# Kernel tuning notes

Measured on AMD Instinct MI355X. Metric: run time of the kernel, lower is better.

## Reference

```python
import jax, jax.numpy as jnp
import numpy as np

L, D, H, V, B, S = 12, 768, 12, 50257, 1, 2048
F = 4 * D
HD = D // H
EPS = 1e-5
NEG = -1e38


def setup_inputs() -> dict:
    key = jax.random.key(0)
    ks = jax.random.split(key, 12)
    s = 0.02
    f32 = jnp.float32
    return {
        "x": jax.random.normal(ks[0], (B, S, D), f32),
        "ln1_g": jnp.ones((L, D), f32), "ln1_b": jnp.zeros((L, D), f32),
        "Wq": jax.random.normal(ks[1], (L, D, D), f32) * s,
        "Wk": jax.random.normal(ks[2], (L, D, D), f32) * s,
        "Wv": jax.random.normal(ks[3], (L, D, D), f32) * s,
        "Wo": jax.random.normal(ks[4], (L, D, D), f32) * s,
        "bo": jnp.zeros((L, D), f32),
        "ln2_g": jnp.ones((L, D), f32), "ln2_b": jnp.zeros((L, D), f32),
        "Wfc": jax.random.normal(ks[5], (L, D, F), f32) * s,
        "bfc": jnp.zeros((L, F), f32),
        "Wp": jax.random.normal(ks[6], (L, F, D), f32) * s,
        "bp": jnp.zeros((L, D), f32),
        "lnf_g": jnp.ones((D,), f32), "lnf_b": jnp.zeros((D,), f32),
        "Wlm": jax.random.normal(ks[7], (D, V), f32) * s,
    }


def _ln(h, g, b):
    mu = h.mean(-1, keepdims=True)
    var = ((h - mu) ** 2).mean(-1, keepdims=True)
    return (h - mu) * jax.lax.rsqrt(var + EPS) * g + b


def reference(x, ln1_g, ln1_b, Wq, Wk, Wv, Wo, bo, ln2_g, ln2_b,
              Wfc, bfc, Wp, bp, lnf_g, lnf_b, Wlm):
    Bx, Sx, Dx = x.shape
    # additive causal mask, NOTE: original has no 1/sqrt(head_dim) scaling
    mask = (1.0 - jnp.tril(jnp.ones((Sx, Sx), x.dtype))) * NEG

    def block(h, p):
        g1, b1, wq, wk, wv, wo, bo_, g2, b2, wfc, bfc_, wp, bp_ = p
        hn = _ln(h, g1, b1)
        def heads(w):  # [B,S,D] -> [B,H,S,hd]
            return (hn @ w).reshape(Bx, Sx, H, HD).transpose(0, 2, 1, 3)
        q, k, v = heads(wq), heads(wk), heads(wv)
        scores = jnp.einsum('bhqd,bhkd->bhqk', q, k) + mask
        probs = jax.nn.softmax(scores, axis=-1)
        attn = jnp.einsum('bhqk,bhkd->bhqd', probs, v)
        attn = attn.transpose(0, 2, 1, 3).reshape(Bx, Sx, Dx)
        h = h + attn @ wo + bo_
        hn2 = _ln(h, g2, b2)
        ff = jax.nn.gelu(hn2 @ wfc + bfc_, approximate=False) @ wp + bp_
        return h + ff, None

    h, _ = jax.lax.scan(
        block, x,
        (ln1_g, ln1_b, Wq, Wk, Wv, Wo, bo, ln2_g, ln2_b, Wfc, bfc, Wp, bp))
    return _ln(h, lnf_g, lnf_b) @ Wlm
```

## Files before the change

kernel.cpp:

```cpp
#include <hip/hip_runtime.h>
#include <hip/hip_bf16.h>
#include <math.h>

typedef unsigned short ushort;
typedef __attribute__((ext_vector_type(8))) short short8;
typedef __attribute__((ext_vector_type(4))) short short4v;
typedef __attribute__((ext_vector_type(4))) float f4v;

constexpr int SEQ = 2048;
constexpr int DM  = 768;
constexpr int NH  = 12;
constexpr int HDM = 64;
constexpr int FF  = 3072;
constexpr int NL  = 12;
constexpr int NV  = 50257;
constexpr int NVP = 50304;

__device__ inline ushort f2bf(float f) {
    union { float f; unsigned u; } v; v.f = f;
    unsigned r = v.u + 0x7fffu + ((v.u >> 16) & 1u);
    return (ushort)(r >> 16);
}

__device__ __forceinline__ void gld16(const ushort* g, ushort* l) {
    __builtin_amdgcn_global_load_lds(
        (const __attribute__((address_space(1))) void*)g,
        (__attribute__((address_space(3))) void*)l, 16, 0, 0);
}

__global__ __launch_bounds__(256) void ln_kernel(const float* __restrict__ x,
                                                 const float* __restrict__ g,
                                                 const float* __restrict__ b,
                                                 ushort* __restrict__ out) {
    int row = blockIdx.x;
    int t = threadIdx.x;
    const float* xr = x + (size_t)row * DM;
    float v0 = xr[t], v1 = xr[t + 256], v2 = xr[t + 512];
    float s = v0 + v1 + v2;
    float s2 = v0 * v0 + v1 * v1 + v2 * v2;
    for (int m = 1; m < 64; m <<= 1) { s += __shfl_xor(s, m); s2 += __shfl_xor(s2, m); }
    __shared__ float ls[4], ls2[4];
    int w = t >> 6;
    if ((t & 63) == 0) { ls[w] = s; ls2[w] = s2; }
    __syncthreads();
    s = ls[0] + ls[1] + ls[2] + ls[3];
    s2 = ls2[0] + ls2[1] + ls2[2] + ls2[3];
    float mu = s * (1.0f / DM);
    float var = s2 * (1.0f / DM) - mu * mu;
    float rs = rsqrtf(var + 1e-5f);
    ushort* o = out + (size_t)row * DM;
    o[t]       = f2bf((v0 - mu) * rs * g[t]       + b[t]);
    o[t + 256] = f2bf((v1 - mu) * rs * g[t + 256] + b[t + 256]);
    o[t + 512] = f2bf((v2 - mu) * rs * g[t + 512] + b[t + 512]);
}

__global__ __launch_bounds__(256) void cvt_t(const float* __restrict__ in, size_t inL,
                                             ushort* __restrict__ out, size_t outL,
                                             int K, int N) {
    __shared__ ushort T[64][72];
    int l = blockIdx.z;
    const float* ip = in + (size_t)l * inL;
    ushort* op = out + (size_t)l * outL;
    int kb = blockIdx.x * 64, nb = blockIdx.y * 64;
    int t = threadIdx.x;
    int nl = t & 63, ks = (t >> 6) * 16;
    int n = nb + nl;
    #pragma unroll
    for (int j = 0; j < 16; ++j) {
        float f = (n < N) ? ip[(size_t)(kb + ks + j) * N + n] : 0.f;
        T[nl][ks + j] = f2bf(f);
    }
    __syncthreads();
    int r = t >> 2, c4 = (t & 3) * 16;
    *(short8*)(op + (size_t)(nb + r) * K + kb + c4)     = *(const short8*)&T[r][c4];
    *(short8*)(op + (size_t)(nb + r) * K + kb + c4 + 8) = *(const short8*)&T[r][c4 + 8];
}

template <int BM, int BN, int EPI, bool DB>
__global__ __launch_bounds__(256) void gemmT(const ushort* __restrict__ A,
                                             const ushort* __restrict__ Bt,
                                             const float* __restrict__ bias,
                                             const float* __restrict__ res,
                                             void* __restrict__ outp,
                                             ushort* __restrict__ vt,
                                             int M, int N, int K, int ldOut) {
    constexpr int FM = BM / 32;
    constexpr int FN = BN / 32;
    constexpr int NBUF = DB ? 2 : 1;
    constexpr int ASZ = BM * 64;
    constexpr int BSZ = BN * 64;
    __shared__ ushort As[NBUF * ASZ];
    __shared__ ushort Bs[NBUF * BSZ];
    int tid = threadIdx.x, lane = tid & 63, wave = tid >> 6;
    int wm = (wave >> 1) * (BM / 2), wn = (wave & 1) * (BN / 2);
    int mBase = blockIdx.x * BM, nBase = blockIdx.y * BN;
    int lr = lane & 15, lg = lane >> 4;
    int swz = (lr & 7) << 3;

    f4v acc[FM][FN];
    #pragma unroll
    for (int i = 0; i < FM; ++i)
        #pragma unroll
        for (int j = 0; j < FN; ++j) acc[i][j] = (f4v){0.f, 0.f, 0.f, 0.f};

    int cBase = wave * 64 + lane;

    auto stage = [&](int kb, int buf) {
        #pragma unroll
        for (int i = 0; i < BM / 32; ++i) {
            int c = i * 256 + cBase;
            int row = c >> 3;
            int kc = (c & 7) ^ (row & 7);
            gld16(A + (size_t)(mBase + row) * K + kb + kc * 8,
                  As + buf * ASZ + (size_t)(i * 256 + wave * 64) * 8);
        }
        #pragma unroll
        for (int i = 0; i < BN / 32; ++i) {
            int c = i * 256 + cBase;
            int row = c >> 3;
            int kc = (c & 7) ^ (row & 7);
            gld16(Bt + (size_t)(nBase + row) * K + kb + kc * 8,
                  Bs + buf * BSZ + (size_t)(i * 256 + wave * 64) * 8);
        }
    };
    auto compute = [&](int buf) {
        #pragma unroll
        for (int kk = 0; kk < 2; ++kk) {
            short8 a[FM], b[FN];
            #pragma unroll
            for (int fr = 0; fr < FM; ++fr)
                a[fr] = *(const short8*)(As + buf * ASZ + (wm + fr * 16 + lr) * 64 + ((((kk * 4 + lg) << 3)) ^ swz));
            #pragma unroll
            for (int fc = 0; fc < FN; ++fc)
                b[fc] = *(const short8*)(Bs + buf * BSZ + (wn + fc * 16 + lr) * 64 + ((((kk * 4 + lg) << 3)) ^ swz));
            #pragma unroll
            for (int fr = 0; fr < FM; ++fr)
                #pragma unroll
                for (int fc = 0; fc < FN; ++fc)
                    acc[fr][fc] = __builtin_amdgcn_mfma_f32_16x16x32_bf16(a[fr], b[fc], acc[fr][fc], 0, 0, 0);
        }
    };

    if constexpr (DB) {
        stage(0, 0);
        __syncthreads();
        int cur = 0;
        for (int kb = 0; kb < K; kb += 64) {
            if (kb + 64 < K) stage(kb + 64, cur ^ 1);
            compute(cur);
            __syncthreads();
            cur ^= 1;
        }
    } else {
        for (int kb = 0; kb < K; kb += 64) {
            stage(kb, 0);
            __syncthreads();
            compute(0);
            __syncthreads();
        }
    }

    if constexpr (EPI == 4) {
        if (nBase < 1536) {
            #pragma unroll
            for (int fr = 0; fr < FM; ++fr)
                #pragma unroll
                for (int fc = 0; fc < FN; ++fc)
                    #pragma unroll
                    for (int r = 0; r < 4; ++r) {
                        int row = mBase + wm + fr * 16 + 4 * lg + r;
                        int col = nBase + wn + fc * 16 + lr;
                        ((ushort*)outp)[(size_t)row * ldOut + col] = f2bf(acc[fr][fc][r]);
                    }
        } else {
            #pragma unroll
            for (int fr = 0; fr < FM; ++fr)
                #pragma unroll
                for (int fc = 0; fc < FN; ++fc) {
                    short4v pk;
                    #pragma unroll
                    for (int r = 0; r < 4; ++r) pk[r] = (short)f2bf(acc[fr][fc][r]);
                    int d  = nBase - 1536 + wn + fc * 16 + lr;
                    int m0 = mBase + wm + fr * 16 + 4 * lg;
                    *(short4v*)(vt + (size_t)d * SEQ + m0) = pk;
                }
        }
        return;
    }

    #pragma unroll
    for (int fr = 0; fr < FM; ++fr)
        #pragma unroll
        for (int fc = 0; fc < FN; ++fc)
            #pragma unroll
            for (int r = 0; r < 4; ++r) {
                int row = mBase + wm + fr * 16 + 4 * lg + r;
                int col = nBase + wn + fc * 16 + lr;
                float v = acc[fr][fc][r];
                if constexpr (EPI == 0) {
                    ((ushort*)outp)[(size_t)row * ldOut + col] = f2bf(v);
                } else if constexpr (EPI == 1) {
                    v += bias[col] + res[(size_t)row * ldOut + col];
                    ((float*)outp)[(size_t)row * ldOut + col] = v;
                } else if constexpr (EPI == 2) {
                    v += bias[col];
                    v = 0.5f * v * (1.f + erff(v * 0.70710678118f));
                    ((ushort*)outp)[(size_t)row * ldOut + col] = f2bf(v);
                } else {
                    if (col < N) ((float*)outp)[(size_t)row * ldOut + col] = v;
                }
            }
}

__global__ __launch_bounds__(256) void attn_v6(const ushort* __restrict__ Qg,
                                               const ushort* __restrict__ Kg,
                                               const ushort* __restrict__ Vt,
                                               ushort* __restrict__ Og) {
    __shared__ ushort Ks[2 * 4096];
    __shared__ ushort Vs[2 * 4096];
    __shared__ ushort Ps[4 * 16 * 64];
    int tid = threadIdx.x, lane = tid & 63, wave = tid >> 6;
    int flat = blockIdx.x;
    int qb   = (SEQ / 64) - 1 - (flat / NH);
    int head = flat % NH;
    int lr = lane & 15, lg = lane >> 4;
    int qr0 = qb * 64 + wave * 16;
    int hoff = head * HDM;
    int swz = (lr & 7) << 3;

    short8 qf0 = *(const short8*)(Qg + (size_t)(qr0 + lr) * 2304 + hoff + lg * 8);
    short8 qf1 = *(const short8*)(Qg + (size_t)(qr0 + lr) * 2304 + hoff + 32 + lg * 8);

    const f4v fz = {0.f, 0.f, 0.f, 0.f};
    f4v o[4];
    o[0] = fz; o[1] = fz; o[2] = fz; o[3] = fz;
    float mrow[4] = {-1e30f, -1e30f, -1e30f, -1e30f};
    float lsum[4] = {0.f, 0.f, 0.f, 0.f};

    int c0 = wave * 64 + lane;
    int c1 = c0 + 256;
    int r0 = c0 >> 3, kc0 = ((c0 & 7) ^ (r0 & 7)) * 8;
    int r1 = c1 >> 3, kc1 = ((c1 & 7) ^ (r1 & 7)) * 8;

    auto stageKV = [&](int kb, int buf) {
        gld16(Kg + (size_t)(kb * 64 + r0) * 2304 + hoff + kc0, Ks + buf * 4096 + wave * 512);
        gld16(Kg + (size_t)(kb * 64 + r1) * 2304 + hoff + kc1, Ks + buf * 4096 + 2048 + wave * 512);
        gld16(Vt + (size_t)(hoff + r0) * SEQ + kb * 64 + kc0,  Vs + buf * 4096 + wave * 512);
        gld16(Vt + (size_t)(hoff + r1) * SEQ + kb * 64 + kc1,  Vs + buf * 4096 + 2048 + wave * 512);
    };

    stageKV(0, 0);
    __syncthreads();
    int cur = 0;

    for (int kb = 0; kb <= qb; ++kb) {
        if (kb < qb) stageKV(kb + 1, cur ^ 1);

        f4v s[4];
        #pragma unroll
        for (int n = 0; n < 4; ++n) {
            const ushort* kr = Ks + cur * 4096 + (n * 16 + lr) * 64;
            short8 k0 = *(const short8*)(kr + ((lg << 3) ^ swz));
            short8 k1 = *(const short8*)(kr + ((((4 + lg) << 3)) ^ swz));
            f4v z = fz;
            z = __builtin_amdgcn_mfma_f32_16x16x32_bf16(qf0, k0, z, 0, 0, 0);
            s[n] = __builtin_amdgcn_mfma_f32_16x16x32_bf16(qf1, k1, z, 0, 0, 0);
        }
        if (kb == qb) {
            #pragma unroll
            for (int n = 0; n < 4; ++n)
                #pragma unroll
                for (int r = 0; r < 4; ++r) {
                    int col = kb * 64 + n * 16 + lr;
                    int row = qr0 + 4 * lg + r;
                    if (col > row) s[n][r] = -1e38f;
                }
        }

        int sub = lr & 7, hi = lr >> 3;
        #pragma unroll
        for (int r = 0; r < 4; ++r) {
            float mx = fmaxf(fmaxf(s[0][r], s[1][r]), fmaxf(s[2][r], s[3][r]));
            mx = fmaxf(mx, __shfl_xor(mx, 1));
            mx = fmaxf(mx, __shfl_xor(mx, 2));
            mx = fmaxf(mx, __shfl_xor(mx, 4));
            mx = fmaxf(mx, __shfl_xor(mx, 8));
            float mnew = fmaxf(mrow[r], mx);
            float corr = __expf(mrow[r] - mnew);
            float ps0 = __expf(s[0][r] - mnew);
            float ps1 = __expf(s[1][r] - mnew);
            float ps2 = __expf(s[2][r] - mnew);
            float ps3 = __expf(s[3][r] - mnew);
            float rs = ps0 + ps1 + ps2 + ps3;
            rs += __shfl_xor(rs, 1);
            rs += __shfl_xor(rs, 2);
            rs += __shfl_xor(rs, 4);
            rs += __shfl_xor(rs, 8);
            lsum[r] = lsum[r] * corr + rs;
            mrow[r] = mnew;
            o[0][r] *= corr; o[1][r] *= corr; o[2][r] *= corr; o[3][r] *= corr;
            int prow = 4 * lg + r;
            ushort* pb = Ps + wave * 1024 + prow * 64;
            int px = prow & 7;
            pb[(((0 + hi) ^ px) << 3) | sub] = f2bf(ps0);
            pb[(((2 + hi) ^ px) << 3) | sub] = f2bf(ps1);
            pb[(((4 + hi) ^ px) << 3) | sub] = f2bf(ps2);
            pb[(((6 + hi) ^ px) << 3) | sub] = f2bf(ps3);
        }
        __syncthreads();

        #pragma unroll
        for (int kk = 0; kk < 2; ++kk) {
            short8 pa = *(const short8*)(Ps + wave * 1024 + lr * 64 + ((((kk * 4 + lg) << 3)) ^ swz));
            #pragma unroll
            for (int dn = 0; dn < 4; ++dn) {
                short8 vb = *(const short8*)(Vs + cur * 4096 + (dn * 16 + lr) * 64 + ((((kk * 4 + lg) << 3)) ^ swz));
                o[dn] = __builtin_amdgcn_mfma_f32_16x16x32_bf16(pa, vb, o[dn], 0, 0, 0);
            }
        }
        __syncthreads();
        cur ^= 1;
    }

    #pragma unroll
    for (int dn = 0; dn < 4; ++dn)
        #pragma unroll
        for (int r = 0; r < 4; ++r) {
            int row = qr0 + 4 * lg + r;
            Og[(size_t)row * DM + hoff + dn * 16 + lr] = f2bf(o[dn][r] / lsum[r]);
        }
}

template <int EPI>
__global__ __launch_bounds__(256) void gemm64(const ushort* __restrict__ A,
                                              const float* __restrict__ B,
                                              const float* __restrict__ bias,
                                              const float* __restrict__ res,
                                              void* __restrict__ outp,
                                              int M, int N, int K) {
    __shared__ ushort As[64][64];
    __shared__ ushort Bs[64][72];
    int tid = threadIdx.x;
    int lane = tid & 63, wave = tid >> 6;
    int wm = (wave >> 1) * 32, wn = (wave & 1) * 32;
    int mBase = blockIdx.x * 64, nBase = blockIdx.y * 64;
    int lr = lane & 15, lg = lane >> 4;

    const f4v fz = {0.f, 0.f, 0.f, 0.f};
    f4v acc[2][2];
    acc[0][0] = fz; acc[0][1] = fz; acc[1][0] = fz; acc[1][1] = fz;

    int ar = tid >> 2, ac = (tid & 3) * 16;
    int br = tid >> 2, bc = (tid & 3) * 16;

    for (int kb = 0; kb < K; kb += 64) {
        const short8* ag = (const short8*)(A + (size_t)(mBase + ar) * K + kb + ac);
        *(short8*)&As[ar][ac]     = ag[0];
        *(short8*)&As[ar][ac + 8] = ag[1];
        if constexpr (EPI == 3) {
            #pragma unroll
            for (int j = 0; j < 16; ++j) {
                int col = nBase + bc + j;
                float f = (col < N) ? B[(size_t)(kb + br) * N + col] : 0.f;
                Bs[bc + j][br] = f2bf(f);
            }
        } else {
            const float4* bg = (const float4*)(B + (size_t)(kb + br) * N + nBase + bc);
            float fv[16];
            *(float4*)&fv[0]  = bg[0];
            *(float4*)&fv[4]  = bg[1];
            *(float4*)&fv[8]  = bg[2];
            *(float4*)&fv[12] = bg[3];
            #pragma unroll
            for (int j = 0; j < 16; ++j) Bs[bc + j][br] = f2bf(fv[j]);
        }
        __syncthreads();
        #pragma unroll
        for (int kk = 0; kk < 2; ++kk) {
            short8 a0 = *(const short8*)&As[wm + lr][kk * 32 + lg * 8];
            short8 a1 = *(const short8*)&As[wm + 16 + lr][kk * 32 + lg * 8];
            short8 b0 = *(const short8*)&Bs[wn + lr][kk * 32 + lg * 8];
            short8 b1 = *(const short8*)&Bs[wn + 16 + lr][kk * 32 + lg * 8];
            acc[0][0] = __builtin_amdgcn_mfma_f32_16x16x32_bf16(a0, b0, acc[0][0], 0, 0, 0);
            acc[0][1] = __builtin_amdgcn_mfma_f32_16x16x32_bf16(a0, b1, acc[0][1], 0, 0, 0);
            acc[1][0] = __builtin_amdgcn_mfma_f32_16x16x32_bf16(a1, b0, acc[1][0], 0, 0, 0);
            acc[1][1] = __builtin_amdgcn_mfma_f32_16x16x32_bf16(a1, b1, acc[1][1], 0, 0, 0);
        }
        __syncthreads();
    }

    #pragma unroll
    for (int fm = 0; fm < 2; ++fm)
        #pragma unroll
        for (int fn = 0; fn < 2; ++fn)
            #pragma unroll
            for (int r = 0; r < 4; ++r) {
                int row = mBase + wm + fm * 16 + 4 * lg + r;
                int col = nBase + wn + fn * 16 + lr;
                float v = acc[fm][fn][r];
                if constexpr (EPI == 0) {
                    ((ushort*)outp)[(size_t)row * N + col] = f2bf(v);
                } else if constexpr (EPI == 1) {
                    v += bias[col] + res[(size_t)row * N + col];
                    ((float*)outp)[(size_t)row * N + col] = v;
                } else if constexpr (EPI == 2) {
                    v += bias[col];
                    v = 0.5f * v * (1.f + erff(v * 0.70710678118f));
                    ((ushort*)outp)[(size_t)row * N + col] = f2bf(v);
                } else {
                    if (col < N) ((float*)outp)[(size_t)row * N + col] = v;
                }
            }
}

__global__ __launch_bounds__(256) void attn_stage(const ushort* __restrict__ Qg,
                                                  const ushort* __restrict__ Kg,
                                                  const ushort* __restrict__ Vg,
                                                  ushort* __restrict__ Og,
                                                  int ld) {
    __shared__ ushort Ks[64][64];
    __shared__ ushort Vs[64][72];
    __shared__ ushort Ps[4][16][64];
    int tid = threadIdx.x, lane = tid & 63, wave = tid >> 6;
    int qb = blockIdx.x, head = blockIdx.y;
    int lr = lane & 15, lg = lane >> 4;
    int qr0 = qb * 64 + wave * 16;
    size_t hoff = (size_t)head * HDM;

    short8 qf0 = *(const short8*)(Qg + (size_t)(qr0 + lr) * ld + hoff + lg * 8);
    short8 qf1 = *(const short8*)(Qg + (size_t)(qr0 + lr) * ld + hoff + 32 + lg * 8);

    const f4v fz = {0.f, 0.f, 0.f, 0.f};
    f4v o[4];
    o[0] = fz; o[1] = fz; o[2] = fz; o[3] = fz;
    float mrow[4] = {-1e30f, -1e30f, -1e30f, -1e30f};
    float lsum[4] = {0.f, 0.f, 0.f, 0.f};

    int r_ = tid >> 2, c_ = (tid & 3) * 16;

    for (int kb = 0; kb <= qb; ++kb) {
        const short8* kg = (const short8*)(Kg + (size_t)(kb * 64 + r_) * ld + hoff + c_);
        *(short8*)&Ks[r_][c_]     = kg[0];
        *(short8*)&Ks[r_][c_ + 8] = kg[1];
        const short8* vg = (const short8*)(Vg + (size_t)(kb * 64 + r_) * ld + hoff + c_);
        short8 v0 = vg[0], v1 = vg[1];
        #pragma unroll
        for (int j = 0; j < 8; ++j) {
            Vs[c_ + j][r_]     = (ushort)v0[j];
            Vs[c_ + 8 + j][r_] = (ushort)v1[j];
        }
        __syncthreads();

        f4v s[4];
        #pragma unroll
        for (int n = 0; n < 4; ++n) {
            short8 k0 = *(const short8*)&Ks[n * 16 + lr][lg * 8];
            short8 k1 = *(const short8*)&Ks[n * 16 + lr][32 + lg * 8];
            f4v z = fz;
            z = __builtin_amdgcn_mfma_f32_16x16x32_bf16(qf0, k0, z, 0, 0, 0);
            s[n] = __builtin_amdgcn_mfma_f32_16x16x32_bf16(qf1, k1, z, 0, 0, 0);
        }
        if (kb == qb) {
            #pragma unroll
            for (int n = 0; n < 4; ++n)
                #pragma unroll
                for (int r = 0; r < 4; ++r) {
                    int col = kb * 64 + n * 16 + lr;
                    int row = qr0 + 4 * lg + r;
                    if (col > row) s[n][r] = -1e38f;
                }
        }

        #pragma unroll
        for (int r = 0; r < 4; ++r) {
            float mx = fmaxf(fmaxf(s[0][r], s[1][r]), fmaxf(s[2][r], s[3][r]));
            mx = fmaxf(mx, __shfl_xor(mx, 1));
            mx = fmaxf(mx, __shfl_xor(mx, 2));
            mx = fmaxf(mx, __shfl_xor(mx, 4));
            mx = fmaxf(mx, __shfl_xor(mx, 8));
            float mnew = fmaxf(mrow[r], mx);
            float corr = __expf(mrow[r] - mnew);
            float ps0 = __expf(s[0][r] - mnew);
            float ps1 = __expf(s[1][r] - mnew);
            float ps2 = __expf(s[2][r] - mnew);
            float ps3 = __expf(s[3][r] - mnew);
            float rs = ps0 + ps1 + ps2 + ps3;
            rs += __shfl_xor(rs, 1);
            rs += __shfl_xor(rs, 2);
            rs += __shfl_xor(rs, 4);
            rs += __shfl_xor(rs, 8);
            lsum[r] = lsum[r] * corr + rs;
            mrow[r] = mnew;
            o[0][r] *= corr; o[1][r] *= corr; o[2][r] *= corr; o[3][r] *= corr;
            Ps[wave][4 * lg + r][0 * 16 + lr] = f2bf(ps0);
            Ps[wave][4 * lg + r][1 * 16 + lr] = f2bf(ps1);
            Ps[wave][4 * lg + r][2 * 16 + lr] = f2bf(ps2);
            Ps[wave][4 * lg + r][3 * 16 + lr] = f2bf(ps3);
        }
        __syncthreads();

        #pragma unroll
        for (int kk = 0; kk < 2; ++kk) {
            short8 pa = *(const short8*)&Ps[wave][lr][kk * 32 + lg * 8];
            #pragma unroll
            for (int dn = 0; dn < 4; ++dn) {
                short8 vb = *(const short8*)&Vs[dn * 16 + lr][kk * 32 + lg * 8];
                o[dn] = __builtin_amdgcn_mfma_f32_16x16x32_bf16(pa, vb, o[dn], 0, 0, 0);
            }
        }
        __syncthreads();
    }

    #pragma unroll
    for (int dn = 0; dn < 4; ++dn)
        #pragma unroll
        for (int r = 0; r < 4; ++r) {
            int row = qr0 + 4 * lg + r;
            Og[(size_t)row * DM + hoff + dn * 16 + lr] = f2bf(o[dn][r] / lsum[r]);
        }
}

extern "C" void kernel_launch(void* const* d_in, const int* in_sizes, int n_in,
                              void* d_out, int out_size, void* d_ws, size_t ws_size,
                              hipStream_t stream) {
    const float* x     = (const float*)d_in[0];
    const float* ln1_g = (const float*)d_in[1];
    const float* ln1_b = (const float*)d_in[2];
    const float* Wq    = (const float*)d_in[3];
    const float* Wk    = (const float*)d_in[4];
    const float* Wv    = (const float*)d_in[5];
    const float* Wo    = (const float*)d_in[6];
    const float* bo    = (const float*)d_in[7];
    const float* ln2_g = (const float*)d_in[8];
    const float* ln2_b = (const float*)d_in[9];
    const float* Wfc   = (const float*)d_in[10];
    const float* bfc   = (const float*)d_in[11];
    const float* Wp    = (const float*)d_in[12];
    const float* bp    = (const float*)d_in[13];
    const float* lnf_g = (const float*)d_in[14];
    const float* lnf_b = (const float*)d_in[15];
    const float* Wlm   = (const float*)d_in[16];

    dim3 blk(256);

    size_t offs[12];
    size_t need = 0;
    size_t sizes[11] = {
        (size_t)SEQ * DM * 4,
        (size_t)SEQ * DM * 2,
        (size_t)SEQ * 2304 * 2,
        (size_t)SEQ * DM * 2,
        (size_t)SEQ * FF * 2,
        (size_t)DM * SEQ * 2,
        (size_t)NL * 2304 * DM * 2,
        (size_t)NL * DM * DM * 2,
        (size_t)NL * FF * DM * 2,
        (size_t)NL * DM * FF * 2,
        (size_t)NVP * DM * 2,
    };
    for (int i = 0; i < 11; ++i) { offs[i] = need; need += sizes[i]; }
    offs[11] = need;

    if (ws_size >= need) {
        char* ws = (char*)d_ws;
        float*  h    = (float*)(ws + offs[0]);
        ushort* hn   = (ushort*)(ws + offs[1]);
        ushort* qkv  = (ushort*)(ws + offs[2]);
        ushort* ab_  = (ushort*)(ws + offs[3]);
        ushort* fb_  = (ushort*)(ws + offs[4]);
        ushort* vt   = (ushort*)(ws + offs[5]);
        ushort* qkvw = (ushort*)(ws + offs[6]);
        ushort* wow  = (ushort*)(ws + offs[7]);
        ushort* fcw  = (ushort*)(ws + offs[8]);
        ushort* wpw  = (ushort*)(ws + offs[9]);
        ushort* lmw  = (ushort*)(ws + offs[10]);

        hipMemcpyAsync(h, x, (size_t)SEQ * DM * 4, hipMemcpyDeviceToDevice, stream);

        cvt_t<<<dim3(12, 12, NL), blk, 0, stream>>>(Wq, (size_t)DM * DM, qkvw,               (size_t)2304 * DM, DM, DM);
        cvt_t<<<dim3(12, 12, NL), blk, 0, stream>>>(Wk, (size_t)DM * DM, qkvw + DM * DM,     (size_t)2304 * DM, DM, DM);
        cvt_t<<<dim3(12, 12, NL), blk, 0, stream>>>(Wv, (size_t)DM * DM, qkvw + 2 * DM * DM, (size_t)2304 * DM, DM, DM);
        cvt_t<<<dim3(12, 12, NL), blk, 0, stream>>>(Wo, (size_t)DM * DM, wow, (size_t)DM * DM, DM, DM);
        cvt_t<<<dim3(12, 48, NL), blk, 0, stream>>>(Wfc, (size_t)DM * FF, fcw, (size_t)FF * DM, DM, FF);
        cvt_t<<<dim3(48, 12, NL), blk, 0, stream>>>(Wp,  (size_t)FF * DM, wpw, (size_t)DM * FF, FF, DM);
        cvt_t<<<dim3(12, 786, 1), blk, 0, stream>>>(Wlm, 0, lmw, 0, DM, NV);

        for (int l = 0; l < NL; ++l) {
            const ushort* qw = qkvw + (size_t)l * 2304 * DM;
            ln_kernel<<<SEQ, blk, 0, stream>>>(h, ln1_g + l * DM, ln1_b + l * DM, hn);
            gemmT<128, 128, 4, true><<<dim3(16, 18), blk, 0, stream>>>(hn, qw, nullptr, nullptr, qkv, vt, SEQ, 2304, DM, 2304);
            attn_v6<<<dim3((SEQ / 64) * NH), blk, 0, stream>>>(qkv, qkv + 768, vt, ab_);
            gemmT<128, 64, 1, true><<<dim3(16, 12), blk, 0, stream>>>(ab_, wow + (size_t)l * DM * DM, bo + l * DM, h, h, nullptr, SEQ, DM, DM, DM);
            ln_kernel<<<SEQ, blk, 0, stream>>>(h, ln2_g + l * DM, ln2_b + l * DM, hn);
            gemmT<128, 128, 2, true><<<dim3(16, 24), blk, 0, stream>>>(hn, fcw + (size_t)l * FF * DM, bfc + l * FF, nullptr, fb_, nullptr, SEQ, FF, DM, FF);
            gemmT<128, 64, 1, true><<<dim3(16, 12), blk, 0, stream>>>(fb_, wpw + (size_t)l * DM * FF, bp + l * DM, h, h, nullptr, SEQ, DM, FF, DM);
        }
        ln_kernel<<<SEQ, blk, 0, stream>>>(h, lnf_g, lnf_b, hn);
        gemmT<128, 128, 3, false><<<dim3(16, NVP / 128), blk, 0, stream>>>(hn, lmw, nullptr, nullptr, d_out, nullptr, SEQ, NV, DM, NV);
        return;
    }

    char* ws = (char*)d_ws;
    float*  h   = (float*)ws;   ws += (size_t)SEQ * DM * 4;
    ushort* hn  = (ushort*)ws;  ws += (size_t)SEQ * DM * 2;
    ushort* qb_ = (ushort*)ws;  ws += (size_t)SEQ * DM * 2;
    ushort* kb_ = (ushort*)ws;  ws += (size_t)SEQ * DM * 2;
    ushort* vb_ = (ushort*)ws;  ws += (size_t)SEQ * DM * 2;
    ushort* ab_ = (ushort*)ws;  ws += (size_t)SEQ * DM * 2;
    ushort* fb_ = (ushort*)ws;  ws += (size_t)SEQ * FF * 2;

    hipMemcpyAsync(h, x, (size_t)SEQ * DM * 4, hipMemcpyDeviceToDevice, stream);

    dim3 gdd(SEQ / 64, DM / 64);
    dim3 gdf(SEQ / 64, FF / 64);
    dim3 gda(SEQ / 64, NH);
    dim3 gdl(SEQ / 64, (NV + 63) / 64);

    for (int l = 0; l < NL; ++l) {
        ln_kernel<<<SEQ, blk, 0, stream>>>(h, ln1_g + l * DM, ln1_b + l * DM, hn);
        gemm64<0><<<gdd, blk, 0, stream>>>(hn, Wq + (size_t)l * DM * DM, nullptr, nullptr, qb_, SEQ, DM, DM);
        gemm64<0><<<gdd, blk, 0, stream>>>(hn, Wk + (size_t)l * DM * DM, nullptr, nullptr, kb_, SEQ, DM, DM);
        gemm64<0><<<gdd, blk, 0, stream>>>(hn, Wv + (size_t)l * DM * DM, nullptr, nullptr, vb_, SEQ, DM, DM);
        attn_stage<<<gda, blk, 0, stream>>>(qb_, kb_, vb_, ab_, DM);
        gemm64<1><<<gdd, blk, 0, stream>>>(ab_, Wo + (size_t)l * DM * DM, bo + l * DM, h, h, SEQ, DM, DM);
        ln_kernel<<<SEQ, blk, 0, stream>>>(h, ln2_g + l * DM, ln2_b + l * DM, hn);
        gemm64<2><<<gdf, blk, 0, stream>>>(hn, Wfc + (size_t)l * DM * FF, bfc + l * FF, nullptr, fb_, SEQ, FF, DM);
        gemm64<1><<<gdd, blk, 0, stream>>>(fb_, Wp + (size_t)l * FF * DM, bp + l * DM, h, h, SEQ, DM, FF);
    }
    ln_kernel<<<SEQ, blk, 0, stream>>>(h, lnf_g, lnf_b, hn);
    gemm64<3><<<gdl, blk, 0, stream>>>(hn, Wlm, nullptr, nullptr, d_out, SEQ, NV, DM);
}
```

Measured before the change: 2.648 ms.

## Fuse weight conversions, shrink layer GEMM tiles, swizzle LM-head blocks across XCDs

Merges the seven weight-conversion launches into one segmented kernel to cut launch overhead. Shrinks the per-layer GEMM tiles from 128x128/128x64 to 64x64 so the small GEMMs launch more workgroups and fill the GPU's many CUs. The LM-head GEMM now double-buffers its shared-memory staging and remaps workgroup IDs so neighbouring tiles land on the same XCD for better L2 reuse. Smaller tiles give less data reuse per block and may raise global memory traffic.

```diff
diff --git a/kernel.cpp b/kernel.cpp
--- a/kernel.cpp
+++ b/kernel.cpp
@@ -54,14 +54,30 @@
     o[t + 512] = f2bf((v2 - mu) * rs * g[t + 512] + b[t + 512]);
 }
 
-__global__ __launch_bounds__(256) void cvt_t(const float* __restrict__ in, size_t inL,
-                                             ushort* __restrict__ out, size_t outL,
-                                             int K, int N) {
+struct CvtArgs {
+    const float* src[7];
+    ushort*      dst[7];
+    long inL[7], outL[7];
+    int  K[7], N[7], tk[7], tn[7];
+    int  base[8];
+};
+
+__global__ __launch_bounds__(256) void cvt_all(CvtArgs a) {
     __shared__ ushort T[64][72];
-    int l = blockIdx.z;
-    const float* ip = in + (size_t)l * inL;
-    ushort* op = out + (size_t)l * outL;
-    int kb = blockIdx.x * 64, nb = blockIdx.y * 64;
+    int idx = blockIdx.x;
+    int seg = 0;
+    #pragma unroll
+    for (int i = 1; i < 7; ++i) if (idx >= a.base[i]) seg = i;
+    int local = idx - a.base[seg];
+    int K = a.K[seg], N = a.N[seg];
+    int tk = a.tk[seg], tn = a.tn[seg];
+    int k_t = local % tk;
+    int rst = local / tk;
+    int n_t = rst % tn;
+    int l   = rst / tn;
+    const float* ip = a.src[seg] + (size_t)l * a.inL[seg];
+    ushort* op      = a.dst[seg] + (size_t)l * a.outL[seg];
+    int kb = k_t * 64, nb = n_t * 64;
     int t = threadIdx.x;
     int nl = t & 63, ks = (t >> 6) * 16;
     int n = nb + nl;
@@ -76,7 +92,7 @@
     *(short8*)(op + (size_t)(nb + r) * K + kb + c4 + 8) = *(const short8*)&T[r][c4 + 8];
 }
 
-template <int BM, int BN, int EPI, bool DB>
+template <int BM, int BN, int EPI, bool DB, bool SWZ>
 __global__ __launch_bounds__(256) void gemmT(const ushort* __restrict__ A,
                                              const ushort* __restrict__ Bt,
                                              const float* __restrict__ bias,
@@ -93,7 +109,20 @@
     __shared__ ushort Bs[NBUF * BSZ];
     int tid = threadIdx.x, lane = tid & 63, wave = tid >> 6;
     int wm = (wave >> 1) * (BM / 2), wn = (wave & 1) * (BN / 2);
-    int mBase = blockIdx.x * BM, nBase = blockIdx.y * BN;
+    int mBase, nBase;
+    if constexpr (SWZ) {
+        int gx = gridDim.x;
+        int nwg = gx * gridDim.y;
+        int flat = blockIdx.y * gx + blockIdx.x;
+        int xcd = flat & 7, idx = flat >> 3;
+        int q = nwg >> 3, r = nwg & 7;
+        int wg = (xcd < r ? xcd * (q + 1) : r * (q + 1) + (xcd - r) * q) + idx;
+        mBase = (wg % gx) * BM;
+        nBase = (wg / gx) * BN;
+    } else {
+        mBase = blockIdx.x * BM;
+        nBase = blockIdx.y * BN;
+    }
     int lr = lane & 15, lg = lane >> 4;
     int swz = (lr & 7) << 3;
 
@@ -577,26 +606,41 @@
 
         hipMemcpyAsync(h, x, (size_t)SEQ * DM * 4, hipMemcpyDeviceToDevice, stream);
 
-        cvt_t<<<dim3(12, 12, NL), blk, 0, stream>>>(Wq, (size_t)DM * DM, qkvw,               (size_t)2304 * DM, DM, DM);
-        cvt_t<<<dim3(12, 12, NL), blk, 0, stream>>>(Wk, (size_t)DM * DM, qkvw + DM * DM,     (size_t)2304 * DM, DM, DM);
-        cvt_t<<<dim3(12, 12, NL), blk, 0, stream>>>(Wv, (size_t)DM * DM, qkvw + 2 * DM * DM, (size_t)2304 * DM, DM, DM);
-        cvt_t<<<dim3(12, 12, NL), blk, 0, stream>>>(Wo, (size_t)DM * DM, wow, (size_t)DM * DM, DM, DM);
-        cvt_t<<<dim3(12, 48, NL), blk, 0, stream>>>(Wfc, (size_t)DM * FF, fcw, (size_t)FF * DM, DM, FF);
-        cvt_t<<<dim3(48, 12, NL), blk, 0, stream>>>(Wp,  (size_t)FF * DM, wpw, (size_t)DM * FF, FF, DM);
-        cvt_t<<<dim3(12, 786, 1), blk, 0, stream>>>(Wlm, 0, lmw, 0, DM, NV);
+        CvtArgs ca;
+        const float* srcs[7] = {Wq, Wk, Wv, Wo, Wfc, Wp, Wlm};
+        ushort* dsts[7] = {qkvw, qkvw + DM * DM, qkvw + 2 * DM * DM, wow, fcw, wpw, lmw};
+        long inLs[7]  = {(long)DM * DM, (long)DM * DM, (long)DM * DM, (long)DM * DM,
+                         (long)DM * FF, (long)FF * DM, 0};
+        long outLs[7] = {(long)2304 * DM, (long)2304 * DM, (long)2304 * DM, (long)DM * DM,
+                         (long)FF * DM, (long)DM * FF, 0};
+        int Ks_[7] = {DM, DM, DM, DM, DM, FF, DM};
+        int Ns_[7] = {DM, DM, DM, DM, FF, DM, NV};
+        int tks[7] = {12, 12, 12, 12, 12, 48, 12};
+        int tns[7] = {12, 12, 12, 12, 48, 12, 786};
+        int lays[7] = {NL, NL, NL, NL, NL, NL, 1};
+        int total = 0;
+        for (int i = 0; i < 7; ++i) {
+            ca.src[i] = srcs[i]; ca.dst[i] = dsts[i];
+            ca.inL[i] = inLs[i]; ca.outL[i] = outLs[i];
+            ca.K[i] = Ks_[i]; ca.N[i] = Ns_[i]; ca.tk[i] = tks[i]; ca.tn[i] = tns[i];
+            ca.base[i] = total;
+            total += tks[i] * tns[i] * lays[i];
+        }
+        ca.base[7] = total;
+        cvt_all<<<dim3(total), blk, 0, stream>>>(ca);
 
         for (int l = 0; l < NL; ++l) {
             const ushort* qw = qkvw + (size_t)l * 2304 * DM;
             ln_kernel<<<SEQ, blk, 0, stream>>>(h, ln1_g + l * DM, ln1_b + l * DM, hn);
-            gemmT<128, 128, 4, true><<<dim3(16, 18), blk, 0, stream>>>(hn, qw, nullptr, nullptr, qkv, vt, SEQ, 2304, DM, 2304);
+            gemmT<64, 64, 4, true, false><<<dim3(32, 36), blk, 0, stream>>>(hn, qw, nullptr, nullptr, qkv, vt, SEQ, 2304, DM, 2304);
             attn_v6<<<dim3((SEQ / 64) * NH), blk, 0, stream>>>(qkv, qkv + 768, vt, ab_);
-            gemmT<128, 64, 1, true><<<dim3(16, 12), blk, 0, stream>>>(ab_, wow + (size_t)l * DM * DM, bo + l * DM, h, h, nullptr, SEQ, DM, DM, DM);
+            gemmT<64, 64, 1, true, false><<<dim3(32, 12), blk, 0, stream>>>(ab_, wow + (size_t)l * DM * DM, bo + l * DM, h, h, nullptr, SEQ, DM, DM, DM);
             ln_kernel<<<SEQ, blk, 0, stream>>>(h, ln2_g + l * DM, ln2_b + l * DM, hn);
-            gemmT<128, 128, 2, true><<<dim3(16, 24), blk, 0, stream>>>(hn, fcw + (size_t)l * FF * DM, bfc + l * FF, nullptr, fb_, nullptr, SEQ, FF, DM, FF);
-            gemmT<128, 64, 1, true><<<dim3(16, 12), blk, 0, stream>>>(fb_, wpw + (size_t)l * DM * FF, bp + l * DM, h, h, nullptr, SEQ, DM, FF, DM);
+            gemmT<64, 64, 2, true, false><<<dim3(32, 48), blk, 0, stream>>>(hn, fcw + (size_t)l * FF * DM, bfc + l * FF, nullptr, fb_, nullptr, SEQ, FF, DM, FF);
+            gemmT<64, 64, 1, true, false><<<dim3(32, 12), blk, 0, stream>>>(fb_, wpw + (size_t)l * DM * FF, bp + l * DM, h, h, nullptr, SEQ, DM, FF, DM);
         }
         ln_kernel<<<SEQ, blk, 0, stream>>>(h, lnf_g, lnf_b, hn);
-        gemmT<128, 128, 3, false><<<dim3(16, NVP / 128), blk, 0, stream>>>(hn, lmw, nullptr, nullptr, d_out, nullptr, SEQ, NV, DM, NV);
+        gemmT<128, 128, 3, true, true><<<dim3(16, NVP / 128), blk, 0, stream>>>(hn, lmw, nullptr, nullptr, d_out, nullptr, SEQ, NV, DM, NV);
         return;
     }
 
```

New measurement: 2.605 ms. Within noise of the previous version (-1.6%).
